# Kernel tuning notes

Hardware: AMD Instinct MI355X
Metric: run time of the kernel (lower is better)

## Reference

```python
import jax, jax.numpy as jnp
import numpy as np
import math

MODEL_DIM = 1024
BATCH = 4
SEQ = 4096
ATTENTION_INPUT = 'both'


def make_F(model_dim, attention_input):
    F = jnp.zeros((model_dim, model_dim), dtype=jnp.float32)
    if attention_input == 'both':
        a = model_dim
    else:
        a = model_dim // 2
    # faithful to source: elif means 'both' only hits the first branch
    if attention_input in ['both', 'only_sem']:
        idx = jnp.arange(0, a)
        F = F.at[idx, idx].set(1.0)
    elif attention_input in ['only_pos']:
        idx = jnp.arange(a, 2 * a)
        F = F.at[idx, idx].set(1.0)
    return F


def setup_inputs() -> dict:
    key = jax.random.key(0)
    kx, kq, kk, kv = jax.random.split(key, 4)
    x = jax.random.normal(kx, (BATCH, SEQ, MODEL_DIM), dtype=jnp.float32)
    Q = jax.random.normal(kq, (MODEL_DIM, MODEL_DIM), dtype=jnp.float32) / math.sqrt(MODEL_DIM)
    K = jax.random.normal(kk, (MODEL_DIM, MODEL_DIM), dtype=jnp.float32) / math.sqrt(MODEL_DIM)
    V = jax.random.normal(kv, (MODEL_DIM, MODEL_DIM), dtype=jnp.float32) / math.sqrt(MODEL_DIM)
    return {"x": x, "Q": Q, "K": K, "V": V}


def reference(x, Q, K, V):
    model_dim = Q.shape[0]
    F = make_F(model_dim, ATTENTION_INPUT)
    Qx = x @ F @ Q            # [B, S, D]
    Kx = x @ F @ K            # [B, S, D]
    Vx = x @ V                # [B, S, D]
    scores = jnp.einsum('bqd,bkd->bqk', Qx, Kx) / math.sqrt(model_dim)  # [B, S, S]
    seq = x.shape[1]
    causal_mask = jnp.triu(jnp.ones((seq, seq), dtype=bool), k=1)       # True above diagonal
    scores = jnp.where(causal_mask, -jnp.inf, scores)
    probs = jax.nn.softmax(scores, axis=-1)
    return jnp.einsum('bqk,bkd->bqd', probs, Vx)
```

## Files before the change

### kernel.cpp

```cpp
#include <hip/hip_runtime.h>
#include <cstdint>
#include <cstddef>
#include <cmath>


typedef unsigned short u16;
typedef __bf16  bf16x8 __attribute__((ext_vector_type(8)));
typedef float   f32x4  __attribute__((ext_vector_type(4)));
typedef unsigned short u16x4 __attribute__((ext_vector_type(4)));
typedef unsigned short u16x8 __attribute__((ext_vector_type(8)));

typedef __attribute__((address_space(1))) void gvoid;
typedef __attribute__((address_space(3))) void lvoid;

__device__ __forceinline__ u16 f2bf(float f) {
  union { float f; unsigned u; } v; v.f = f;
  unsigned u = v.u;
  u += 0x7FFFu + ((u >> 16) & 1u);
  return (u16)(u >> 16);
}
__device__ __forceinline__ float bf2f(u16 h) {
  union { unsigned u; float f; } v; v.u = ((unsigned)h) << 16;
  return v.f;
}
__device__ __forceinline__ void async16(const void* g, void* l) {
  __builtin_amdgcn_global_load_lds((gvoid*)(void*)g, (lvoid*)l, 16, 0, 0);
}

__global__ void __launch_bounds__(256) cvt_f32_bf16(const float4* __restrict__ in,
                                                    u16* __restrict__ out, int n4) {
  int i = blockIdx.x * 256 + threadIdx.x;
  if (i >= n4) return;
  float4 v = in[i];
  u16x4 o = { f2bf(v.x), f2bf(v.y), f2bf(v.z), f2bf(v.w) };
  *(u16x4*)(out + 4 * (size_t)i) = o;
}

template <typename TIN>
__global__ void __launch_bounds__(256) transpose_to_bf16(
    const TIN* __restrict__ in, u16* __restrict__ out,
    int rows, int cols, long inStride, long outStride, float scale) {
  __shared__ u16 t[64][68];
  int rt = blockIdx.x * 64, ct = blockIdx.y * 64;
  long ib = (long)blockIdx.z * inStride, ob = (long)blockIdx.z * outStride;
  int tx = threadIdx.x & 63, ty = threadIdx.x >> 6;
#pragma unroll
  for (int r = ty; r < 64; r += 4)
    t[r][tx] = f2bf((float)in[ib + (long)(rt + r) * cols + ct + tx] * scale);
  __syncthreads();
#pragma unroll
  for (int r = ty; r < 64; r += 4)
    out[ob + (long)(ct + r) * rows + rt + tx] = t[tx][r];
}


#define G8_BAR()  __builtin_amdgcn_s_barrier()
#define G8_VMC4() asm volatile("s_waitcnt vmcnt(4)" ::: "memory")
#define G8_VMC0() asm volatile("s_waitcnt vmcnt(0)" ::: "memory")

#define G8_STAGE_A(bn, kp, kb) do { \
    async16(Ag + (kb) + a0, (void*)&As[bn][kp][l0]); \
    async16(Ag + (kb) + a1, (void*)&As[bn][kp][l1]); } while (0)
#define G8_STAGE_B(bn, kp, kb) do { \
    async16(Bg + (kb) + b0, (void*)&Bs[bn][kp][l0]); \
    async16(Bg + (kb) + b1, (void*)&Bs[bn][kp][l1]); } while (0)

#define G8_LDA(bc, kp, ch) do { _Pragma("unroll") \
    for (int u_ = 0; u_ < 4; ++u_) \
      af[u_] = *(const bf16x8*)&As[bc][kp][(wm * 128 + (ch) * 64 + u_ * 16 + lr) * 32 + swq]; \
  } while (0)
#define G8_LDB(bc, kp) do { _Pragma("unroll") \
    for (int j_ = 0; j_ < 4; ++j_) \
      bf[j_] = *(const bf16x8*)&Bs[bc][kp][(wn * 64 + j_ * 16 + lr) * 32 + swq]; \
  } while (0)

#define G8_MFMA(ch) do { \
    __builtin_amdgcn_s_setprio(1); \
    _Pragma("unroll") for (int u_ = 0; u_ < 4; ++u_) \
      _Pragma("unroll") for (int j_ = 0; j_ < 4; ++j_) \
        acc[(ch) * 4 + u_][j_] = __builtin_amdgcn_mfma_f32_16x16x32_bf16( \
            af[u_], bf[j_], acc[(ch) * 4 + u_][j_], 0, 0, 0); \
    __builtin_amdgcn_s_setprio(0); } while (0)

#define G8_TILE(bc, bn, kn) do { \
    bf16x8 af[4], bf[4]; \
    G8_LDB(bc, 0); G8_LDA(bc, 0, 0); \
    G8_STAGE_A(bn, 0, (kn)); \
    G8_BAR(); G8_MFMA(0); G8_BAR(); \
    G8_LDA(bc, 0, 1); \
    G8_STAGE_B(bn, 0, (kn)); \
    G8_BAR(); G8_MFMA(1); G8_VMC4(); G8_BAR(); \
    G8_LDB(bc, 1); G8_LDA(bc, 1, 0); \
    G8_STAGE_A(bn, 1, (kn) + 32); \
    G8_BAR(); G8_MFMA(0); G8_BAR(); \
    G8_LDA(bc, 1, 1); \
    G8_STAGE_B(bn, 1, (kn) + 32); \
    G8_BAR(); G8_MFMA(1); G8_VMC4(); G8_BAR(); } while (0)

template <bool OUTF32>
__global__ void __launch_bounds__(512, 2) gemm8_bt(
    const u16* __restrict__ A, const u16* __restrict__ Bt, void* __restrict__ C,
    int K, int lda, int ldb, int ldc,
    long aStride, long bStride, long cStride, float alpha) {
  const int mt = blockIdx.x, nt = blockIdx.y, bz = blockIdx.z;
  const int tid = threadIdx.x, wv = tid >> 6, ln = tid & 63;
  const int wm = wv & 1, wn = wv >> 1;
  const int lr = ln & 15, quad = ln >> 4;
  const int swq = (quad ^ ((lr >> 1) & 3)) << 3;
  const u16* Ag = A + (long)bz * aStride + (long)(mt * 256) * lda;
  const u16* Bg = Bt + (long)bz * bStride + (long)(nt * 256) * ldb;

  __shared__ __align__(16) __bf16 As[2][2][256 * 32];
  __shared__ __align__(16) __bf16 Bs[2][2][256 * 32];

  f32x4 acc[8][4];
#pragma unroll
  for (int i = 0; i < 8; ++i)
#pragma unroll
    for (int j = 0; j < 4; ++j)
#pragma unroll
      for (int r = 0; r < 4; ++r) acc[i][j][r] = 0.f;

  const int c0 = tid, c1 = tid + 512;
  const int r0 = c0 >> 2, r1 = c1 >> 2;
  const long a0 = (long)r0 * lda + (((c0 & 3) ^ ((r0 >> 1) & 3)) << 3);
  const long a1 = (long)r1 * lda + (((c1 & 3) ^ ((r1 >> 1) & 3)) << 3);
  const long b0 = (long)r0 * ldb + (((c0 & 3) ^ ((r0 >> 1) & 3)) << 3);
  const long b1 = (long)r1 * ldb + (((c1 & 3) ^ ((r1 >> 1) & 3)) << 3);
  const int l0 = c0 * 8, l1 = c1 * 8;

  const int kend = K;

  G8_STAGE_A(0, 0, 0); G8_STAGE_B(0, 0, 0);
  G8_STAGE_A(0, 1, 32); G8_STAGE_B(0, 1, 32);
  G8_VMC4(); G8_BAR();

  for (int k0 = 0; k0 < kend; k0 += 128) {
    const long kn0 = (k0 + 64  < kend) ? (long)k0 + 64  : (long)k0;
    const long kn1 = (k0 + 128 < kend) ? (long)k0 + 128 : (long)k0 + 64;
    G8_TILE(0, 1, kn0);
    G8_TILE(1, 0, kn1);
  }
  G8_VMC0();

  const long cb = (long)bz * cStride;
#pragma unroll
  for (int i = 0; i < 8; ++i) {
    int row0 = mt * 256 + wm * 128 + i * 16 + quad * 4;
#pragma unroll
    for (int j = 0; j < 4; ++j) {
      int col = nt * 256 + wn * 64 + j * 16 + lr;
#pragma unroll
      for (int r = 0; r < 4; ++r) {
        float v = acc[i][j][r] * alpha;
        long idx = cb + (long)(row0 + r) * ldc + col;
        if (OUTF32) ((float*)C)[idx] = v;
        else        ((u16*)C)[idx]  = f2bf(v);
      }
    }
  }
}

template <bool OUTF32, bool TRI, bool CK, int BM>
__global__ void __launch_bounds__(256, BM == 256 ? 3 : 5) gemm_bt(
    const u16* __restrict__ A, const u16* __restrict__ Bt, void* __restrict__ C,
    int K, int lda, int ldb, int ldc,
    long aStride, long bStride, long cStride, float alpha) {
  constexpr int MR = BM / 32;
  constexpr int AQ = BM / 64;
  int mt, nt, bz;
  if (TRI) {
    const int bid = blockIdx.x;
    int m = (int)((sqrtf(4.0f * (float)bid + 1.0f) - 1.0f) * 0.5f);
    while ((m + 1) * (m + 2) <= bid) ++m;
    while (m * (m + 1) > bid) --m;
    mt = m; nt = bid - m * (m + 1);
    bz = blockIdx.z;
  } else if (CK) {
    const int id = blockIdx.x;
    const int g = id & 7, mid = (id >> 3) & 31, hi = id >> 8;
    bz = mid & 3; nt = mid >> 2;
    mt = (hi == 0) ? 31 - g : (hi == 1) ? 16 + g : (hi == 2) ? 15 - g : g;
  } else {
    mt = blockIdx.x; nt = blockIdx.y; bz = blockIdx.z;
  }
  const int tid = threadIdx.x, wv = tid >> 6, ln = tid & 63;
  const u16* Ag = A + (long)bz * aStride + (long)(mt * BM) * lda;
  const u16* Bg = Bt + (long)bz * bStride + (long)(nt * 128) * ldb;

  __shared__ __align__(16) __bf16 As[2][BM * 32];
  __shared__ __align__(16) __bf16 Bs[2][128 * 32];

  f32x4 acc[MR][4];
#pragma unroll
  for (int i = 0; i < MR; ++i)
#pragma unroll
    for (int j = 0; j < 4; ++j)
#pragma unroll
      for (int r = 0; r < 4; ++r) acc[i][j][r] = 0.f;

  const int kend = CK ? (((mt + 1) * BM < K) ? (mt + 1) * BM : K) : K;
  const int wm = wv & 1, wn = wv >> 1;
  const int mrow = wm * (BM / 2), nrow = wn * 64;
  const int lr = ln & 15, quad = ln >> 4;

  long aOff[AQ]; int aLds[AQ];
#pragma unroll
  for (int q = 0; q < AQ; ++q) {
    int c = q * 256 + tid, row = c >> 2, c8i = c & 3;
    aOff[q] = (long)row * lda + ((c8i ^ ((row >> 1) & 3)) << 3);
    aLds[q] = c * 8;
  }
  long bOff[2]; int bLds[2];
#pragma unroll
  for (int q = 0; q < 2; ++q) {
    int c = q * 256 + tid, row = c >> 2, c8i = c & 3;
    bOff[q] = (long)row * ldb + ((c8i ^ ((row >> 1) & 3)) << 3);
    bLds[q] = c * 8;
  }
  const int swq = (quad ^ ((lr >> 1) & 3)) << 3;

  for (int k0 = 0; k0 < kend; k0 += 64) {
#pragma unroll
    for (int p = 0; p < 2; ++p) {
      const long kk = k0 + p * 32;
#pragma unroll
      for (int q = 0; q < AQ; ++q)
        async16(Ag + kk + aOff[q], (char*)As[p] + aLds[q] * 2);
#pragma unroll
      for (int q = 0; q < 2; ++q)
        async16(Bg + kk + bOff[q], (char*)Bs[p] + bLds[q] * 2);
    }
    __syncthreads();
#pragma unroll
    for (int p = 0; p < 2; ++p) {
      bf16x8 af[MR], bfr[4];
#pragma unroll
      for (int u = 0; u < MR; ++u)
        af[u] = *(const bf16x8*)&As[p][(mrow + u * 16 + lr) * 32 + swq];
#pragma unroll
      for (int j = 0; j < 4; ++j)
        bfr[j] = *(const bf16x8*)&Bs[p][(nrow + j * 16 + lr) * 32 + swq];
#pragma unroll
      for (int u = 0; u < MR; ++u)
#pragma unroll
        for (int j = 0; j < 4; ++j)
          acc[u][j] = __builtin_amdgcn_mfma_f32_16x16x32_bf16(af[u], bfr[j], acc[u][j], 0, 0, 0);
    }
    __syncthreads();
  }

  const long cb = (long)bz * cStride;
#pragma unroll
  for (int i = 0; i < MR; ++i) {
    int row0 = mt * BM + mrow + i * 16 + quad * 4;
#pragma unroll
    for (int j = 0; j < 4; ++j) {
      int col = nt * 128 + nrow + j * 16 + lr;
#pragma unroll
      for (int r = 0; r < 4; ++r) {
        float v = acc[i][j][r] * alpha;
        long idx = cb + (long)(row0 + r) * ldc + col;
        if (OUTF32) ((float*)C)[idx] = v;
        else        ((u16*)C)[idx]  = f2bf(v);
      }
    }
  }
}

__global__ void __launch_bounds__(256) softmax_rows(u16* __restrict__ Sb,
                                                    long bStride, int S) {
  const int row = blockIdx.x;
  u16* p = Sb + (long)blockIdx.y * bStride + (long)row * S;
  const int L = row + 1;
  const int Lpad = (L + 255) & ~255;
  const int tid = threadIdx.x, ln = tid & 63, wv = tid >> 6;
  const int base0 = tid * 16;
  __shared__ float red[4];

  float vals[16];
  float lmax = -3.4e38f;
#pragma unroll
  for (int k = 0; k < 2; ++k) {
    const int b = base0 + k * 8;
    if (b < L) {
      u16x8 v = *(const u16x8*)(p + b);
#pragma unroll
      for (int e = 0; e < 8; ++e) {
        if (b + e < L) { float f = bf2f(v[e]); vals[k * 8 + e] = f; lmax = fmaxf(lmax, f); }
        else vals[k * 8 + e] = 0.f;
      }
    } else {
#pragma unroll
      for (int e = 0; e < 8; ++e) vals[k * 8 + e] = 0.f;
    }
  }
#pragma unroll
  for (int o = 32; o > 0; o >>= 1) lmax = fmaxf(lmax, __shfl_down(lmax, o));
  if (ln == 0) red[wv] = lmax;
  __syncthreads();
  float m = fmaxf(fmaxf(red[0], red[1]), fmaxf(red[2], red[3]));

  float lsum = 0.f;
#pragma unroll
  for (int k = 0; k < 2; ++k) {
    const int b = base0 + k * 8;
#pragma unroll
    for (int e = 0; e < 8; ++e) {
      float ex = (b + e < L) ? __expf(vals[k * 8 + e] - m) : 0.f;
      vals[k * 8 + e] = ex; lsum += ex;
    }
  }
#pragma unroll
  for (int o = 32; o > 0; o >>= 1) lsum += __shfl_down(lsum, o);
  __syncthreads();
  if (ln == 0) red[wv] = lsum;
  __syncthreads();
  float inv = 1.f / (red[0] + red[1] + red[2] + red[3]);
#pragma unroll
  for (int k = 0; k < 2; ++k) {
    const int b = base0 + k * 8;
    if (b < Lpad) {
      u16x8 o;
#pragma unroll
      for (int e = 0; e < 8; ++e) o[e] = f2bf(vals[k * 8 + e] * inv);
      *(u16x8*)(p + b) = o;
    }
  }
}

extern "C" void kernel_launch(void* const* d_in, const int* in_sizes, int n_in,
                              void* d_out, int out_size, void* d_ws, size_t ws_size,
                              hipStream_t stream) {
  const float* x = (const float*)d_in[0];
  const float* Q = (const float*)d_in[1];
  const float* K = (const float*)d_in[2];
  const float* V = (const float*)d_in[3];
  float* out = (float*)d_out;

  constexpr int  Bb = 4, S = 4096, D = 1024;
  constexpr long MB = 1024 * 1024;
  if (ws_size < (size_t)(224 * MB)) return;

  char* ws = (char*)d_ws;
  u16* QKx  = (u16*)(ws);
  u16* Vxt  = (u16*)(ws + 64 * MB);
  u16* Sb   = (u16*)(ws + 96 * MB);
  u16* XB   = (u16*)(ws + 128 * MB);
  u16* WTqk = (u16*)(ws + 160 * MB);
  u16* WTv  = (u16*)(ws + 164 * MB);

  const long SD = (long)S * D, SS = (long)S * S;

  cvt_f32_bf16<<<dim3((Bb * S * D / 4) / 256), 256, 0, stream>>>(
      (const float4*)x, XB, Bb * S * D / 4);

  transpose_to_bf16<float><<<dim3(16, 16, 1), 256, 0, stream>>>(
      Q, WTqk, 1024, 1024, 0, 0, 0.03125f);
  transpose_to_bf16<float><<<dim3(16, 16, 1), 256, 0, stream>>>(
      K, WTqk + 1024 * 1024, 1024, 1024, 0, 0, 1.0f);
  transpose_to_bf16<float><<<dim3(16, 16, 1), 256, 0, stream>>>(
      V, WTv, 1024, 1024, 0, 0, 1.0f);

  gemm8_bt<false><<<dim3(64, 8, 1), 512, 0, stream>>>(
      XB, WTqk, QKx, 1024, 1024, 1024, 2048, 0, 0, 0, 1.0f);
  gemm8_bt<false><<<dim3(4, 64, 1), 512, 0, stream>>>(
      WTv, XB, Vxt, 1024, 1024, 1024, 16384, 0, 0, 0, 1.0f);

  gemm_bt<false, true, false, 256><<<dim3(272, 1, Bb), 256, 0, stream>>>(
      QKx, QKx + 1024, Sb, 1024, 2048, 2048, S, 2 * SD, 2 * SD, SS, 1.0f);

  softmax_rows<<<dim3(S, Bb), 256, 0, stream>>>(Sb, SS, S);

  gemm_bt<true, false, true, 128><<<dim3(1024, 1, 1), 256, 0, stream>>>(
      Sb, Vxt, out, S, S, 16384, D, SS, 4096, SD, 1.0f);
}
```

Baseline: 490.2 us.

## Compute causal QK^T scores with 256x256 gemm8 tiles over a triangular grid

The causal score GEMM now runs on the larger 512-thread gemm8 kernel with 256x256 tiles instead of 256x128 tiles. A new mode maps a 1D grid onto lower-triangular tiles, 136 per batch and 544 in total, over 512 blocks, with the first 32 blocks taking a second tile. The old triangular path is removed from gemm_bt and its launch bound becomes 4 for the remaining PV GEMM. The aim is more data reuse per tile and balanced waves, at the cost of uneven per-block work and less occupancy with the larger kernel.

```diff
diff --git a/kernel.cpp b/kernel.cpp
--- a/kernel.cpp
+++ b/kernel.cpp
@@ -97,29 +97,18 @@
     G8_STAGE_B(bn, 1, (kn) + 32); \
     G8_BAR(); G8_MFMA(1); G8_VMC4(); G8_BAR(); } while (0)
 
-template <bool OUTF32>
+template <bool OUTF32, int MODE>
 __global__ void __launch_bounds__(512, 2) gemm8_bt(
     const u16* __restrict__ A, const u16* __restrict__ Bt, void* __restrict__ C,
     int K, int lda, int ldb, int ldc,
     long aStride, long bStride, long cStride, float alpha) {
-  const int mt = blockIdx.x, nt = blockIdx.y, bz = blockIdx.z;
   const int tid = threadIdx.x, wv = tid >> 6, ln = tid & 63;
   const int wm = wv & 1, wn = wv >> 1;
   const int lr = ln & 15, quad = ln >> 4;
   const int swq = (quad ^ ((lr >> 1) & 3)) << 3;
-  const u16* Ag = A + (long)bz * aStride + (long)(mt * 256) * lda;
-  const u16* Bg = Bt + (long)bz * bStride + (long)(nt * 256) * ldb;
 
   __shared__ __align__(16) __bf16 As[2][2][256 * 32];
   __shared__ __align__(16) __bf16 Bs[2][2][256 * 32];
-
-  f32x4 acc[8][4];
-#pragma unroll
-  for (int i = 0; i < 8; ++i)
-#pragma unroll
-    for (int j = 0; j < 4; ++j)
-#pragma unroll
-      for (int r = 0; r < 4; ++r) acc[i][j][r] = 0.f;
 
   const int c0 = tid, c1 = tid + 512;
   const int r0 = c0 >> 2, r1 = c1 >> 2;
@@ -129,54 +118,79 @@
   const long b1 = (long)r1 * ldb + (((c1 & 3) ^ ((r1 >> 1) & 3)) << 3);
   const int l0 = c0 * 8, l1 = c1 * 8;
 
-  const int kend = K;
-
-  G8_STAGE_A(0, 0, 0); G8_STAGE_B(0, 0, 0);
-  G8_STAGE_A(0, 1, 32); G8_STAGE_B(0, 1, 32);
-  G8_VMC4(); G8_BAR();
-
-  for (int k0 = 0; k0 < kend; k0 += 128) {
-    const long kn0 = (k0 + 64  < kend) ? (long)k0 + 64  : (long)k0;
-    const long kn1 = (k0 + 128 < kend) ? (long)k0 + 128 : (long)k0 + 64;
-    G8_TILE(0, 1, kn0);
-    G8_TILE(1, 0, kn1);
-  }
-  G8_VMC0();
-
-  const long cb = (long)bz * cStride;
-#pragma unroll
-  for (int i = 0; i < 8; ++i) {
-    int row0 = mt * 256 + wm * 128 + i * 16 + quad * 4;
-#pragma unroll
-    for (int j = 0; j < 4; ++j) {
-      int col = nt * 256 + wn * 64 + j * 16 + lr;
-#pragma unroll
-      for (int r = 0; r < 4; ++r) {
-        float v = acc[i][j][r] * alpha;
-        long idx = cb + (long)(row0 + r) * ldc + col;
-        if (OUTF32) ((float*)C)[idx] = v;
-        else        ((u16*)C)[idx]  = f2bf(v);
+  int t0 = 0, t1 = 0, ntile = 1;
+  if (MODE == 1) {
+    const int id = blockIdx.x;
+    if (id < 32) { t0 = id; t1 = 512 + id; ntile = 2; }
+    else         { t0 = id; }
+  }
+
+  for (int tt = 0; tt < ntile; ++tt) {
+    int mt, nt, bz;
+    if (MODE == 1) {
+      const int t = (tt == 0) ? t0 : t1;
+      bz = t / 136;
+      const int r = t - bz * 136;
+      int m = (int)((sqrtf(8.0f * (float)r + 1.0f) - 1.0f) * 0.5f);
+      while ((m + 1) * (m + 2) / 2 <= r) ++m;
+      while (m * (m + 1) / 2 > r) --m;
+      mt = m; nt = r - m * (m + 1) / 2;
+    } else {
+      mt = blockIdx.x; nt = blockIdx.y; bz = blockIdx.z;
+    }
+    const u16* Ag = A + (long)bz * aStride + (long)(mt * 256) * lda;
+    const u16* Bg = Bt + (long)bz * bStride + (long)(nt * 256) * ldb;
+
+    f32x4 acc[8][4];
+#pragma unroll
+    for (int i = 0; i < 8; ++i)
+#pragma unroll
+      for (int j = 0; j < 4; ++j)
+#pragma unroll
+        for (int r = 0; r < 4; ++r) acc[i][j][r] = 0.f;
+
+    const int kend = K;
+
+    G8_STAGE_A(0, 0, 0); G8_STAGE_B(0, 0, 0);
+    G8_STAGE_A(0, 1, 32); G8_STAGE_B(0, 1, 32);
+    G8_VMC4(); G8_BAR();
+
+    for (int k0 = 0; k0 < kend; k0 += 128) {
+      const long kn0 = (k0 + 64  < kend) ? (long)k0 + 64  : (long)k0;
+      const long kn1 = (k0 + 128 < kend) ? (long)k0 + 128 : (long)k0 + 64;
+      G8_TILE(0, 1, kn0);
+      G8_TILE(1, 0, kn1);
+    }
+    G8_VMC0();
+
+    const long cb = (long)bz * cStride;
+#pragma unroll
+    for (int i = 0; i < 8; ++i) {
+      int row0 = mt * 256 + wm * 128 + i * 16 + quad * 4;
+#pragma unroll
+      for (int j = 0; j < 4; ++j) {
+        int col = nt * 256 + wn * 64 + j * 16 + lr;
+#pragma unroll
+        for (int r = 0; r < 4; ++r) {
+          float v = acc[i][j][r] * alpha;
+          long idx = cb + (long)(row0 + r) * ldc + col;
+          if (OUTF32) ((float*)C)[idx] = v;
+          else        ((u16*)C)[idx]  = f2bf(v);
+        }
       }
     }
   }
 }
 
-template <bool OUTF32, bool TRI, bool CK, int BM>
-__global__ void __launch_bounds__(256, BM == 256 ? 3 : 5) gemm_bt(
+template <bool OUTF32, bool CK, int BM>
+__global__ void __launch_bounds__(256, 4) gemm_bt(
     const u16* __restrict__ A, const u16* __restrict__ Bt, void* __restrict__ C,
     int K, int lda, int ldb, int ldc,
     long aStride, long bStride, long cStride, float alpha) {
   constexpr int MR = BM / 32;
   constexpr int AQ = BM / 64;
   int mt, nt, bz;
-  if (TRI) {
-    const int bid = blockIdx.x;
-    int m = (int)((sqrtf(4.0f * (float)bid + 1.0f) - 1.0f) * 0.5f);
-    while ((m + 1) * (m + 2) <= bid) ++m;
-    while (m * (m + 1) > bid) --m;
-    mt = m; nt = bid - m * (m + 1);
-    bz = blockIdx.z;
-  } else if (CK) {
+  if (CK) {
     const int id = blockIdx.x;
     const int g = id & 7, mid = (id >> 3) & 31, hi = id >> 8;
     bz = mid & 3; nt = mid >> 2;
@@ -362,16 +376,16 @@
   transpose_to_bf16<float><<<dim3(16, 16, 1), 256, 0, stream>>>(
       V, WTv, 1024, 1024, 0, 0, 1.0f);
 
-  gemm8_bt<false><<<dim3(64, 8, 1), 512, 0, stream>>>(
+  gemm8_bt<false, 0><<<dim3(64, 8, 1), 512, 0, stream>>>(
       XB, WTqk, QKx, 1024, 1024, 1024, 2048, 0, 0, 0, 1.0f);
-  gemm8_bt<false><<<dim3(4, 64, 1), 512, 0, stream>>>(
+  gemm8_bt<false, 0><<<dim3(4, 64, 1), 512, 0, stream>>>(
       WTv, XB, Vxt, 1024, 1024, 1024, 16384, 0, 0, 0, 1.0f);
 
-  gemm_bt<false, true, false, 256><<<dim3(272, 1, Bb), 256, 0, stream>>>(
+  gemm8_bt<false, 1><<<dim3(512, 1, 1), 512, 0, stream>>>(
       QKx, QKx + 1024, Sb, 1024, 2048, 2048, S, 2 * SD, 2 * SD, SS, 1.0f);
 
   softmax_rows<<<dim3(S, Bb), 256, 0, stream>>>(Sb, SS, S);
 
-  gemm_bt<true, false, true, 128><<<dim3(1024, 1, 1), 256, 0, stream>>>(
+  gemm_bt<true, true, 128><<<dim3(1024, 1, 1), 256, 0, stream>>>(
       Sb, Vxt, out, S, S, 16384, D, SS, 4096, SD, 1.0f);
 }
```

After: 467.2 us. -4.7%, faster.
